# Performance work log

Measured on AMD Instinct MI355X. Metric: run time of the kernel, lower is better.

The kernel has to match this reference:

```python
import jax, jax.numpy as jnp
import numpy as np

BSZ, L, H, P = 8, 4096, 512, 256  # batch, seq len, features, complex state dim (conj_sym)
DT_MIN, DT_MAX = 1e-3, 1e-1


def setup_inputs() -> dict:
    key = jax.random.key(0)
    k_u, k_B, k_C, k_D, k_dt = jax.random.split(key, 5)
    u = jax.random.normal(k_u, (BSZ, L, H), dtype=jnp.float32)
    # HiPPO-like stable init for the diagonal state matrix
    Lambda_re = -0.5 * jnp.ones((P,), dtype=jnp.float32)
    Lambda_im = jnp.pi * jnp.arange(P, dtype=jnp.float32)
    # lecun-normal-ish scaling for real/imag parts of B (fan_in = H) and C (fan_in = P)
    B = jax.random.normal(k_B, (P, H, 2), dtype=jnp.float32) / jnp.sqrt(2.0 * H)
    C = jax.random.normal(k_C, (H, P, 2), dtype=jnp.float32) / jnp.sqrt(2.0 * P)
    D = jax.random.normal(k_D, (H,), dtype=jnp.float32)
    log_step = jax.random.uniform(k_dt, (P, 1), dtype=jnp.float32,
                                  minval=jnp.log(DT_MIN), maxval=jnp.log(DT_MAX))
    return {"u": u, "Lambda_re": Lambda_re, "Lambda_im": Lambda_im,
            "B": B, "C": C, "D": D, "log_step": log_step}


def _binop(q_i, q_j):
    """Associative binary operator for diagonal linear recurrence."""
    A_i, b_i = q_i
    A_j, b_j = q_j
    return (A_j * A_i, A_j * b_i + b_j)


def reference(u, Lambda_re, Lambda_im, B, C, D, log_step):
    # --- setup / discretization (zero-order hold) ---
    Lambda = (Lambda_re + 1j * Lambda_im).astype(jnp.complex64)      # (P,)
    B_tilde = (B[..., 0] + 1j * B[..., 1]).astype(jnp.complex64)     # (P,H)
    C_tilde = (C[..., 0] + 1j * C[..., 1]).astype(jnp.complex64)     # (H,P)
    step = jnp.exp(log_step[:, 0])                                   # (P,)
    Lambda_bar = jnp.exp(Lambda * step)                              # (P,)
    B_bar = ((Lambda_bar - 1.0) / Lambda)[:, None] * B_tilde         # (P,H)

    # --- parallel scan over the sequence (diagonal SSM) ---
    Bu = jnp.einsum('blh,ph->blp', u, B_bar)                         # (B,L,P) complex64
    Lam = jnp.broadcast_to(Lambda_bar, Bu.shape)                     # (B,L,P)
    _, xs = jax.lax.associative_scan(_binop, (Lam, Bu), axis=1)      # (B,L,P)

    # --- emissions (factor 2 from conjugate symmetry) + feedthrough ---
    ys = 2.0 * jnp.einsum('blp,hp->blh', xs, C_tilde).real + D * u   # (B,L,H)
    return jax.nn.gelu(ys)
```

## Files before the change

kernel.cpp:

```cpp
#include <hip/hip_runtime.h>
#include <cstdint>
#include <cstddef>

typedef unsigned short u16;
typedef short short8 __attribute__((ext_vector_type(8)));
typedef float floatx4 __attribute__((ext_vector_type(4)));

#define DEVINL __device__ __forceinline__

static constexpr int BSZ = 8, SEQL = 4096, H = 512, P = 256;
static constexpr int M = BSZ * SEQL;
static constexpr int KD = 512;
static constexpr int ND = 512;
static constexpr int CHUNK = 32;
static constexpr int NCH = SEQL / CHUNK;

DEVINL u16 f2bf(float f) {
  union { float f; unsigned u; } v; v.f = f;
  unsigned r = (v.u + 0x7fffu + ((v.u >> 16) & 1u)) >> 16;
  return (u16)r;
}
DEVINL float bf2f(u16 h) {
  union { unsigned u; float f; } v; v.u = ((unsigned)h) << 16; return v.f;
}

DEVINL void gload_lds16(const u16* g, u16* l) {
  __builtin_amdgcn_global_load_lds(
      (const __attribute__((address_space(1))) unsigned*)g,
      (__attribute__((address_space(3))) unsigned*)l, 16, 0, 0);
}

__global__ void setup_kernel(const float* __restrict__ Lre, const float* __restrict__ Lim,
                             const float* __restrict__ logstep,
                             float2* __restrict__ lam, float2* __restrict__ ffac) {
  int p = threadIdx.x;
  if (p >= P) return;
  float lr = Lre[p], li = Lim[p];
  float st = expf(logstep[p]);
  float mag = expf(lr * st);
  float ang = li * st;
  float cr = mag * cosf(ang);
  float ci = mag * sinf(ang);
  lam[p] = make_float2(cr, ci);
  float a = cr - 1.0f, b = ci;
  float den = lr * lr + li * li;
  float fr = (a * lr + b * li) / den;
  float fi = (b * lr - a * li) / den;
  ffac[p] = make_float2(fr, fi);
}

__global__ void bt1_kernel(const float2* __restrict__ Bin,
                           const float2* __restrict__ ffac,
                           u16* __restrict__ bt1) {
  int idx = blockIdx.x * 256 + threadIdx.x;
  int p = idx / H, h = idx % H;
  float2 bv = Bin[(size_t)p * H + h];
  float2 f = ffac[p];
  float br = f.x * bv.x - f.y * bv.y;
  float bi = f.x * bv.y + f.y * bv.x;
  bt1[(size_t)(2 * p) * H + h]     = f2bf(br);
  bt1[(size_t)(2 * p + 1) * H + h] = f2bf(bi);
}

__global__ void bt2_kernel(const float* __restrict__ Cin, u16* __restrict__ bt2) {
  int idx = blockIdx.x * 256 + threadIdx.x;
  float c = Cin[idx];
  float v = (idx & 1) ? -2.0f * c : 2.0f * c;
  bt2[idx] = f2bf(v);
}

__global__ void ucvt_kernel(const float4* __restrict__ uin, ushort4* __restrict__ ubf) {
  int idx = blockIdx.x * 256 + threadIdx.x;
  float4 f = uin[idx];
  ushort4 o;
  o.x = f2bf(f.x); o.y = f2bf(f.y); o.z = f2bf(f.z); o.w = f2bf(f.w);
  ubf[idx] = o;
}

template <int MODE>
__global__ __launch_bounds__(256, 4) void gemm_bt(const u16* __restrict__ A,
                                                  const u16* __restrict__ Bt,
                                                  u16* __restrict__ outBf,
                                                  float* __restrict__ outF,
                                                  const float* __restrict__ Dv,
                                                  const u16* __restrict__ ubf) {
  __shared__ u16 As[128 * 64];
  __shared__ u16 Bs[128 * 64];
  const int tid = threadIdx.x;
  const int bm = blockIdx.x, bn = blockIdx.y;
  const int wave = tid >> 6, lane = tid & 63;
  const int quad = lane >> 4, l16 = lane & 15;
  const int wm = (wave & 1) << 6, wn = (wave >> 1) << 6;
  const int r7 = l16 & 7;

  floatx4 acc[4][4] = {};

  const u16* Ab = A + (size_t)bm * 128 * KD;
  const u16* Bb = Bt + (size_t)bn * 128 * KD;
  const int srow = tid >> 3;
  const int scol = (((tid & 7) ^ ((tid >> 3) & 7)) << 3);

  for (int k0 = 0; k0 < KD; k0 += 64) {
    __syncthreads();
#pragma unroll
    for (int j = 0; j < 4; j++)
      gload_lds16(Ab + (size_t)(j * 32 + srow) * KD + k0 + scol, &As[j * 2048 + tid * 8]);
#pragma unroll
    for (int j = 0; j < 4; j++)
      gload_lds16(Bb + (size_t)(j * 32 + srow) * KD + k0 + scol, &Bs[j * 2048 + tid * 8]);
    __syncthreads();

#pragma unroll
    for (int h = 0; h < 2; h++) {
      const int pc = (((h << 2) | quad) ^ r7) << 3;
      short8 af[4], bfr[4];
#pragma unroll
      for (int t = 0; t < 4; t++)
        af[t] = *(const short8*)&As[(wm + t * 16 + l16) * 64 + pc];
#pragma unroll
      for (int t = 0; t < 4; t++)
        bfr[t] = *(const short8*)&Bs[(wn + t * 16 + l16) * 64 + pc];
#pragma unroll
      for (int tm = 0; tm < 4; tm++)
#pragma unroll
        for (int tn = 0; tn < 4; tn++)
          acc[tm][tn] = __builtin_amdgcn_mfma_f32_16x16x32_bf16(af[tm], bfr[tn], acc[tm][tn], 0, 0, 0);
    }
  }

  const int row_base = bm * 128 + wm + quad * 4;
  const int col_base = bn * 128 + wn + l16;
  float dv[4];
  if (MODE == 1) {
#pragma unroll
    for (int tn = 0; tn < 4; tn++) dv[tn] = Dv[col_base + tn * 16];
  }
#pragma unroll
  for (int tm = 0; tm < 4; tm++) {
#pragma unroll
    for (int tn = 0; tn < 4; tn++) {
      int n = col_base + tn * 16;
#pragma unroll
      for (int r = 0; r < 4; r++) {
        int m = row_base + tm * 16 + r;
        float v = acc[tm][tn][r];
        if (MODE == 0) {
          outBf[(size_t)m * ND + n] = f2bf(v);
        } else {
          float uv = bf2f(ubf[(size_t)m * ND + n]);
          float ys = v + dv[tn] * uv;
          float y3 = ys * ys * ys;
          float t = tanhf(0.7978845608028654f * (ys + 0.044715f * y3));
          outF[(size_t)m * ND + n] = 0.5f * ys * (1.0f + t);
        }
      }
    }
  }
}

__global__ __launch_bounds__(256) void scan_carry(const u16* __restrict__ Bu,
                                                  const float2* __restrict__ lam,
                                                  float2* __restrict__ carry) {
  int p = threadIdx.x;
  int c = blockIdx.x;
  int b = blockIdx.y;
  float2 lm = lam[p];
  float xr = 0.f, xi = 0.f;
  const u16* base = Bu + ((size_t)b * SEQL + (size_t)c * CHUNK) * 512 + 2 * p;
  for (int l = 0; l < CHUNK; l++) {
    unsigned w = *(const unsigned*)(base + (size_t)l * 512);
    float br = bf2f((u16)(w & 0xffffu));
    float bi = bf2f((u16)(w >> 16));
    float nr = lm.x * xr - lm.y * xi + br;
    float ni = lm.x * xi + lm.y * xr + bi;
    xr = nr; xi = ni;
  }
  carry[((size_t)b * NCH + c) * P + p] = make_float2(xr, xi);
}

__global__ __launch_bounds__(256) void scan_apply(u16* __restrict__ Bu,
                                                  const float2* __restrict__ lam,
                                                  const float2* __restrict__ carry) {
  int p = threadIdx.x;
  int c = blockIdx.x;
  int b = blockIdx.y;
  float2 lm = lam[p];
  float ar = lm.x, ai = lm.y;
#pragma unroll
  for (int i = 0; i < 5; i++) { float nr = ar * ar - ai * ai, ni = 2.f * ar * ai; ar = nr; ai = ni; }
  float xr = 0.f, xi = 0.f;
  for (int j = 0; j < c; j++) {
    float2 ca = carry[((size_t)b * NCH + j) * P + p];
    float nr = ar * xr - ai * xi + ca.x;
    float ni = ar * xi + ai * xr + ca.y;
    xr = nr; xi = ni;
  }
  u16* base = Bu + ((size_t)b * SEQL + (size_t)c * CHUNK) * 512 + 2 * p;
  for (int l = 0; l < CHUNK; l++) {
    unsigned* addr = (unsigned*)(base + (size_t)l * 512);
    unsigned w = *addr;
    float br = bf2f((u16)(w & 0xffffu));
    float bi = bf2f((u16)(w >> 16));
    float nr = lm.x * xr - lm.y * xi + br;
    float ni = lm.x * xi + lm.y * xr + bi;
    xr = nr; xi = ni;
    *addr = (unsigned)f2bf(nr) | ((unsigned)f2bf(ni) << 16);
  }
}

extern "C" void kernel_launch(void* const* d_in, const int* in_sizes, int n_in,
                              void* d_out, int out_size, void* d_ws, size_t ws_size,
                              hipStream_t stream) {
  const float* u      = (const float*)d_in[0];
  const float* Lre    = (const float*)d_in[1];
  const float* Lim    = (const float*)d_in[2];
  const float* Bin    = (const float*)d_in[3];
  const float* Cin    = (const float*)d_in[4];
  const float* Dv     = (const float*)d_in[5];
  const float* lstep  = (const float*)d_in[6];
  float* out          = (float*)d_out;

  char* ws = (char*)d_ws;
  float2* lam    = (float2*)(ws + 0);
  float2* ffac   = (float2*)(ws + 2048);
  u16*    bt1    = (u16*)   (ws + 4096);
  u16*    bt2    = (u16*)   (ws + 528384);
  u16*    ubf    = (u16*)   (ws + 1052672);
  u16*    Bu     = (u16*)   (ws + 34607104);
  float2* carry  = (float2*)(ws + 68161536);

  setup_kernel<<<1, 256, 0, stream>>>(Lre, Lim, lstep, lam, ffac);
  bt1_kernel<<<(P * H) / 256, 256, 0, stream>>>((const float2*)Bin, ffac, bt1);
  bt2_kernel<<<(H * P * 2) / 256, 256, 0, stream>>>(Cin, bt2);
  ucvt_kernel<<<(M * H / 4) / 256, 256, 0, stream>>>((const float4*)u, (ushort4*)ubf);

  gemm_bt<0><<<dim3(M / 128, ND / 128), 256, 0, stream>>>(ubf, bt1, Bu, nullptr, nullptr, nullptr);

  scan_carry<<<dim3(NCH, BSZ), 256, 0, stream>>>(Bu, lam, carry);
  scan_apply<<<dim3(NCH, BSZ), 256, 0, stream>>>(Bu, lam, carry);

  gemm_bt<1><<<dim3(M / 128, ND / 128), 256, 0, stream>>>(Bu, bt2, nullptr, out, Dv, ubf);
}
```

Baseline: 235.3 us.

## Transpose Bu to feature-major layout and add separate chunk-prefix scan kernel

```diff
diff --git a/kernel.cpp b/kernel.cpp
--- a/kernel.cpp
+++ b/kernel.cpp
@@ -83,7 +83,7 @@
                                                   u16* __restrict__ outBf,
                                                   float* __restrict__ outF,
                                                   const float* __restrict__ Dv,
-                                                  const u16* __restrict__ ubf) {
+                                                  const float* __restrict__ u32) {
   __shared__ u16 As[128 * 64];
   __shared__ u16 Bs[128 * 64];
   const int tid = threadIdx.x;
@@ -140,15 +140,19 @@
 #pragma unroll
     for (int tn = 0; tn < 4; tn++) {
       int n = col_base + tn * 16;
-#pragma unroll
-      for (int r = 0; r < 4; r++) {
-        int m = row_base + tm * 16 + r;
-        float v = acc[tm][tn][r];
-        if (MODE == 0) {
-          outBf[(size_t)m * ND + n] = f2bf(v);
-        } else {
-          float uv = bf2f(ubf[(size_t)m * ND + n]);
-          float ys = v + dv[tn] * uv;
+      if (MODE == 0) {
+        int mrow = row_base + tm * 16;
+        ushort4 pk;
+        pk.x = f2bf(acc[tm][tn][0]); pk.y = f2bf(acc[tm][tn][1]);
+        pk.z = f2bf(acc[tm][tn][2]); pk.w = f2bf(acc[tm][tn][3]);
+        size_t addr = ((size_t)(mrow >> 12) * ND + n) * SEQL + (mrow & (SEQL - 1));
+        *(ushort4*)&outBf[addr] = pk;
+      } else {
+#pragma unroll
+        for (int r = 0; r < 4; r++) {
+          int m = row_base + tm * 16 + r;
+          float uv = u32[(size_t)m * ND + n];
+          float ys = acc[tm][tn][r] + dv[tn] * uv;
           float y3 = ys * ys * ys;
           float t = tanhf(0.7978845608028654f * (ys + 0.044715f * y3));
           outF[(size_t)m * ND + n] = 0.5f * ys * (1.0f + t);
@@ -158,19 +162,25 @@
   }
 }
 
-__global__ __launch_bounds__(256) void scan_carry(const u16* __restrict__ Bu,
+__global__ __launch_bounds__(256) void scan_carry(const u16* __restrict__ But,
                                                   const float2* __restrict__ lam,
                                                   float2* __restrict__ carry) {
   int p = threadIdx.x;
   int c = blockIdx.x;
   int b = blockIdx.y;
   float2 lm = lam[p];
+  const u16* rr = But + ((size_t)b * ND + 2 * p) * SEQL + c * CHUNK;
+  const u16* ri = rr + SEQL;
+  short8 rv[4], iv[4];
+#pragma unroll
+  for (int j = 0; j < 4; j++) rv[j] = *(const short8*)(rr + 8 * j);
+#pragma unroll
+  for (int j = 0; j < 4; j++) iv[j] = *(const short8*)(ri + 8 * j);
   float xr = 0.f, xi = 0.f;
-  const u16* base = Bu + ((size_t)b * SEQL + (size_t)c * CHUNK) * 512 + 2 * p;
+#pragma unroll
   for (int l = 0; l < CHUNK; l++) {
-    unsigned w = *(const unsigned*)(base + (size_t)l * 512);
-    float br = bf2f((u16)(w & 0xffffu));
-    float bi = bf2f((u16)(w >> 16));
+    float br = bf2f((u16)rv[l >> 3][l & 7]);
+    float bi = bf2f((u16)iv[l >> 3][l & 7]);
     float nr = lm.x * xr - lm.y * xi + br;
     float ni = lm.x * xi + lm.y * xr + bi;
     xr = nr; xi = ni;
@@ -178,33 +188,51 @@
   carry[((size_t)b * NCH + c) * P + p] = make_float2(xr, xi);
 }
 
-__global__ __launch_bounds__(256) void scan_apply(u16* __restrict__ Bu,
+__global__ __launch_bounds__(256) void scan_prefix(const float2* __restrict__ carry,
+                                                   const float2* __restrict__ lam,
+                                                   float2* __restrict__ prefix) {
+  int p = threadIdx.x;
+  int b = blockIdx.x;
+  float2 lm = lam[p];
+  float ar = lm.x, ai = lm.y;
+#pragma unroll
+  for (int i = 0; i < 5; i++) { float nr = ar * ar - ai * ai, ni = 2.f * ar * ai; ar = nr; ai = ni; }
+  float pr = 0.f, pi = 0.f;
+  for (int c = 0; c < NCH; c++) {
+    prefix[((size_t)b * NCH + c) * P + p] = make_float2(pr, pi);
+    float2 ca = carry[((size_t)b * NCH + c) * P + p];
+    float nr = ar * pr - ai * pi + ca.x;
+    float ni = ar * pi + ai * pr + ca.y;
+    pr = nr; pi = ni;
+  }
+}
+
+__global__ __launch_bounds__(256) void scan_apply(const u16* __restrict__ But,
                                                   const float2* __restrict__ lam,
-                                                  const float2* __restrict__ carry) {
+                                                  const float2* __restrict__ prefix,
+                                                  u16* __restrict__ xs) {
   int p = threadIdx.x;
   int c = blockIdx.x;
   int b = blockIdx.y;
   float2 lm = lam[p];
-  float ar = lm.x, ai = lm.y;
-#pragma unroll
-  for (int i = 0; i < 5; i++) { float nr = ar * ar - ai * ai, ni = 2.f * ar * ai; ar = nr; ai = ni; }
-  float xr = 0.f, xi = 0.f;
-  for (int j = 0; j < c; j++) {
-    float2 ca = carry[((size_t)b * NCH + j) * P + p];
-    float nr = ar * xr - ai * xi + ca.x;
-    float ni = ar * xi + ai * xr + ca.y;
-    xr = nr; xi = ni;
-  }
-  u16* base = Bu + ((size_t)b * SEQL + (size_t)c * CHUNK) * 512 + 2 * p;
+  const u16* rr = But + ((size_t)b * ND + 2 * p) * SEQL + c * CHUNK;
+  const u16* ri = rr + SEQL;
+  short8 rv[4], iv[4];
+#pragma unroll
+  for (int j = 0; j < 4; j++) rv[j] = *(const short8*)(rr + 8 * j);
+#pragma unroll
+  for (int j = 0; j < 4; j++) iv[j] = *(const short8*)(ri + 8 * j);
+  float2 pf = prefix[((size_t)b * NCH + c) * P + p];
+  float xr = pf.x, xi = pf.y;
+  unsigned* orow = (unsigned*)(xs + ((size_t)b * SEQL + (size_t)c * CHUNK) * ND) + p;
+#pragma unroll
   for (int l = 0; l < CHUNK; l++) {
-    unsigned* addr = (unsigned*)(base + (size_t)l * 512);
-    unsigned w = *addr;
-    float br = bf2f((u16)(w & 0xffffu));
-    float bi = bf2f((u16)(w >> 16));
+    float br = bf2f((u16)rv[l >> 3][l & 7]);
+    float bi = bf2f((u16)iv[l >> 3][l & 7]);
     float nr = lm.x * xr - lm.y * xi + br;
     float ni = lm.x * xi + lm.y * xr + bi;
     xr = nr; xi = ni;
-    *addr = (unsigned)f2bf(nr) | ((unsigned)f2bf(ni) << 16);
+    orow[(size_t)l * (ND / 2)] = (unsigned)f2bf(nr) | ((unsigned)f2bf(ni) << 16);
   }
 }
 
@@ -226,18 +254,20 @@
   u16*    bt1    = (u16*)   (ws + 4096);
   u16*    bt2    = (u16*)   (ws + 528384);
   u16*    ubf    = (u16*)   (ws + 1052672);
-  u16*    Bu     = (u16*)   (ws + 34607104);
+  u16*    But    = (u16*)   (ws + 34607104);
   float2* carry  = (float2*)(ws + 68161536);
+  float2* prefix = (float2*)(ws + 70258688);
 
   setup_kernel<<<1, 256, 0, stream>>>(Lre, Lim, lstep, lam, ffac);
   bt1_kernel<<<(P * H) / 256, 256, 0, stream>>>((const float2*)Bin, ffac, bt1);
   bt2_kernel<<<(H * P * 2) / 256, 256, 0, stream>>>(Cin, bt2);
   ucvt_kernel<<<(M * H / 4) / 256, 256, 0, stream>>>((const float4*)u, (ushort4*)ubf);
 
-  gemm_bt<0><<<dim3(M / 128, ND / 128), 256, 0, stream>>>(ubf, bt1, Bu, nullptr, nullptr, nullptr);
-
-  scan_carry<<<dim3(NCH, BSZ), 256, 0, stream>>>(Bu, lam, carry);
-  scan_apply<<<dim3(NCH, BSZ), 256, 0, stream>>>(Bu, lam, carry);
-
-  gemm_bt<1><<<dim3(M / 128, ND / 128), 256, 0, stream>>>(Bu, bt2, nullptr, out, Dv, ubf);
-}
+  gemm_bt<0><<<dim3(M / 128, ND / 128), 256, 0, stream>>>(ubf, bt1, But, nullptr, nullptr, nullptr);
+
+  scan_carry <<<dim3(NCH, BSZ), 256, 0, stream>>>(But, lam, carry);
+  scan_prefix<<<BSZ, 256, 0, stream>>>(carry, lam, prefix);
+  scan_apply <<<dim3(NCH, BSZ), 256, 0, stream>>>(But, lam, prefix, ubf);
+
+  gemm_bt<1><<<dim3(M / 128, ND / 128), 256, 0, stream>>>(ubf, bt2, nullptr, out, Dv, u);
+}
```

After: 242.1 us. 2.9% more time.

## Precompute chunk prefix states in separate kernel instead of per-block serial carry scan

Applied to the files above, without the earlier changes.

```diff
diff --git a/kernel.cpp b/kernel.cpp
--- a/kernel.cpp
+++ b/kernel.cpp
@@ -69,11 +69,13 @@
   bt2[idx] = f2bf(v);
 }
 
-__global__ void ucvt_kernel(const float4* __restrict__ uin, ushort4* __restrict__ ubf) {
+__global__ void ucvt_kernel(const float4* __restrict__ uin, short8* __restrict__ ubf) {
   int idx = blockIdx.x * 256 + threadIdx.x;
-  float4 f = uin[idx];
-  ushort4 o;
-  o.x = f2bf(f.x); o.y = f2bf(f.y); o.z = f2bf(f.z); o.w = f2bf(f.w);
+  float4 f0 = uin[2 * idx];
+  float4 f1 = uin[2 * idx + 1];
+  short8 o;
+  o[0] = f2bf(f0.x); o[1] = f2bf(f0.y); o[2] = f2bf(f0.z); o[3] = f2bf(f0.w);
+  o[4] = f2bf(f1.x); o[5] = f2bf(f1.y); o[6] = f2bf(f1.z); o[7] = f2bf(f1.w);
   ubf[idx] = o;
 }
 
@@ -166,9 +168,10 @@
   int b = blockIdx.y;
   float2 lm = lam[p];
   float xr = 0.f, xi = 0.f;
-  const u16* base = Bu + ((size_t)b * SEQL + (size_t)c * CHUNK) * 512 + 2 * p;
+  const u16* base = Bu + ((size_t)b * SEQL + (size_t)c * CHUNK) * ND + 2 * p;
+#pragma unroll
   for (int l = 0; l < CHUNK; l++) {
-    unsigned w = *(const unsigned*)(base + (size_t)l * 512);
+    unsigned w = *(const unsigned*)(base + (size_t)l * ND);
     float br = bf2f((u16)(w & 0xffffu));
     float bi = bf2f((u16)(w >> 16));
     float nr = lm.x * xr - lm.y * xi + br;
@@ -178,26 +181,38 @@
   carry[((size_t)b * NCH + c) * P + p] = make_float2(xr, xi);
 }
 
+__global__ __launch_bounds__(256) void scan_prefix(const float2* __restrict__ carry,
+                                                   const float2* __restrict__ lam,
+                                                   float2* __restrict__ prefix) {
+  int p = threadIdx.x;
+  int b = blockIdx.x;
+  float2 lm = lam[p];
+  float ar = lm.x, ai = lm.y;
+#pragma unroll
+  for (int i = 0; i < 5; i++) { float nr = ar * ar - ai * ai, ni = 2.f * ar * ai; ar = nr; ai = ni; }
+  float pr = 0.f, pi = 0.f;
+  for (int c = 0; c < NCH; c++) {
+    prefix[((size_t)b * NCH + c) * P + p] = make_float2(pr, pi);
+    float2 ca = carry[((size_t)b * NCH + c) * P + p];
+    float nr = ar * pr - ai * pi + ca.x;
+    float ni = ar * pi + ai * pr + ca.y;
+    pr = nr; pi = ni;
+  }
+}
+
 __global__ __launch_bounds__(256) void scan_apply(u16* __restrict__ Bu,
                                                   const float2* __restrict__ lam,
-                                                  const float2* __restrict__ carry) {
+                                                  const float2* __restrict__ prefix) {
   int p = threadIdx.x;
   int c = blockIdx.x;
   int b = blockIdx.y;
   float2 lm = lam[p];
-  float ar = lm.x, ai = lm.y;
-#pragma unroll
-  for (int i = 0; i < 5; i++) { float nr = ar * ar - ai * ai, ni = 2.f * ar * ai; ar = nr; ai = ni; }
-  float xr = 0.f, xi = 0.f;
-  for (int j = 0; j < c; j++) {
-    float2 ca = carry[((size_t)b * NCH + j) * P + p];
-    float nr = ar * xr - ai * xi + ca.x;
-    float ni = ar * xi + ai * xr + ca.y;
-    xr = nr; xi = ni;
-  }
-  u16* base = Bu + ((size_t)b * SEQL + (size_t)c * CHUNK) * 512 + 2 * p;
+  float2 pf = prefix[((size_t)b * NCH + c) * P + p];
+  float xr = pf.x, xi = pf.y;
+  u16* base = Bu + ((size_t)b * SEQL + (size_t)c * CHUNK) * ND + 2 * p;
+#pragma unroll
   for (int l = 0; l < CHUNK; l++) {
-    unsigned* addr = (unsigned*)(base + (size_t)l * 512);
+    unsigned* addr = (unsigned*)(base + (size_t)l * ND);
     unsigned w = *addr;
     float br = bf2f((u16)(w & 0xffffu));
     float bi = bf2f((u16)(w >> 16));
@@ -228,16 +243,18 @@
   u16*    ubf    = (u16*)   (ws + 1052672);
   u16*    Bu     = (u16*)   (ws + 34607104);
   float2* carry  = (float2*)(ws + 68161536);
+  float2* prefix = (float2*)(ws + 70258688);
 
   setup_kernel<<<1, 256, 0, stream>>>(Lre, Lim, lstep, lam, ffac);
   bt1_kernel<<<(P * H) / 256, 256, 0, stream>>>((const float2*)Bin, ffac, bt1);
   bt2_kernel<<<(H * P * 2) / 256, 256, 0, stream>>>(Cin, bt2);
-  ucvt_kernel<<<(M * H / 4) / 256, 256, 0, stream>>>((const float4*)u, (ushort4*)ubf);
+  ucvt_kernel<<<(M * H / 8) / 256, 256, 0, stream>>>((const float4*)u, (short8*)ubf);
 
   gemm_bt<0><<<dim3(M / 128, ND / 128), 256, 0, stream>>>(ubf, bt1, Bu, nullptr, nullptr, nullptr);
 
-  scan_carry<<<dim3(NCH, BSZ), 256, 0, stream>>>(Bu, lam, carry);
-  scan_apply<<<dim3(NCH, BSZ), 256, 0, stream>>>(Bu, lam, carry);
+  scan_carry <<<dim3(NCH, BSZ), 256, 0, stream>>>(Bu, lam, carry);
+  scan_prefix<<<BSZ, 256, 0, stream>>>(carry, lam, prefix);
+  scan_apply <<<dim3(NCH, BSZ), 256, 0, stream>>>(Bu, lam, prefix);
 
   gemm_bt<1><<<dim3(M / 128, ND / 128), 256, 0, stream>>>(Bu, bt2, nullptr, out, Dv, ubf);
 }
```

Measured after the change: 217.9 us. 7.4% less time.
